# Performance work log

Hardware: AMD Instinct MI355X
Metric: run time of the kernel (lower is better)

## Reference

```python
import jax, jax.numpy as jnp
import numpy as np

TOP_K = 8
NUM_EXPERTS = 64


def setup_inputs() -> dict:
    key = jax.random.key(0)
    k1, k2 = jax.random.split(key)
    x = jax.random.normal(k1, (4, 4096, 2048), dtype=jnp.float32)
    # nn.Linear weight [num_experts, d_model], scaled like typical init
    gate_w = jax.random.normal(k2, (NUM_EXPERTS, 2048), dtype=jnp.float32) * 0.02
    expert_bias = jnp.zeros((NUM_EXPERTS,), dtype=jnp.float32)
    return {"x": x, "gate_w": gate_w, "expert_bias": expert_bias}


def reference(x, gate_w, expert_bias):
    # logits = gate(x): [b, s, E]
    logits = jnp.einsum("bsd,ed->bse", x, gate_w)
    # bias is detached in the original (routing-only, no grad)
    logits_with_bias = logits + jax.lax.stop_gradient(expert_bias)
    # top-k over experts
    top_k_logits, top_k_indices = jax.lax.top_k(logits_with_bias, TOP_K)
    # softmax over the small top-k dimension
    top_k_scores = jax.nn.softmax(top_k_logits, axis=-1)
    # scatter-add load counts per expert (training branch)
    flat_indices = top_k_indices.reshape(-1)
    expert_counts = jnp.zeros((NUM_EXPERTS,), dtype=jnp.int32).at[flat_indices].add(1)
    return top_k_scores, top_k_indices, expert_counts
```

## Files before the change

kernel.cpp:

```cpp
#include <hip/hip_runtime.h>
#include <math.h>

#define DIM   2048
#define NEXP  64
#define TOPK  8
#define ROWS  32
#define NT    512
#define KW    (DIM / 8)
#define STEPS (KW / 16)

typedef __attribute__((ext_vector_type(8)))  short bf16x8;
typedef __attribute__((ext_vector_type(16))) float f32x16;

#define MFMA(A, B, C) __builtin_amdgcn_mfma_f32_32x32x16_bf16(A, B, C, 0, 0, 0)
#define AS_BF(v) (*(const bf16x8*)&(v))

__device__ inline unsigned int bfpack(float a, float b) {
    unsigned int ua = __float_as_uint(a), ub = __float_as_uint(b);
    unsigned int lo = (ua + 0x7FFFu + ((ua >> 16) & 1u)) >> 16;
    unsigned int hi = (ub + 0x7FFFu + ((ub >> 16) & 1u)) & 0xFFFF0000u;
    return hi | lo;
}

__device__ inline void split2pair(float a, float b, unsigned int& h, unsigned int& m) {
    h = bfpack(a, b);
    float ra = a - __uint_as_float(h << 16);
    float rb = b - __uint_as_float(h & 0xFFFF0000u);
    m = bfpack(ra, rb);
}

__global__ __launch_bounds__(256) void prep_kernel(const float* __restrict__ w,
                                                   unsigned int* __restrict__ wpack,
                                                   float* __restrict__ counts) {
    const int t = blockIdx.x * 256 + threadIdx.x;
    if (blockIdx.x == 0 && threadIdx.x < NEXP) counts[threadIdx.x] = 0.0f;
    const float4 v0 = *(const float4*)(w + (size_t)t * 8);
    const float4 v1 = *(const float4*)(w + (size_t)t * 8 + 4);
    unsigned int h[4], m[4];
    split2pair(v0.x, v0.y, h[0], m[0]);
    split2pair(v0.z, v0.w, h[1], m[1]);
    split2pair(v1.x, v1.y, h[2], m[2]);
    split2pair(v1.z, v1.w, h[3], m[3]);
    uint4* dst = (uint4*)(wpack + (size_t)t * 8);
    dst[0] = (uint4){h[0], h[1], h[2], h[3]};
    dst[1] = (uint4){m[0], m[1], m[2], m[3]};
}

__global__ __launch_bounds__(NT, 4) void router_kernel(
    const float* __restrict__ x,
    const unsigned int* __restrict__ wpack,
    const float* __restrict__ bias,
    float* __restrict__ out,
    int M)
{
    __shared__ float lg[8][ROWS][NEXP + 2];
    __shared__ int   hist[NEXP];

    const int tid  = threadIdx.x;
    const int wv   = tid >> 6;
    const int lane = tid & 63;
    const int lrow = lane & 31;
    const int kh   = lane >> 5;
    const int row0 = blockIdx.x * ROWS;
    if (tid < NEXP) hist[tid] = 0;

    const float* xp = x + (size_t)(row0 + lrow) * DIM + wv * KW + kh * 8;
    const unsigned int* wb0 = wpack + ((size_t)lrow * (DIM / 8) + wv * (KW / 8) + kh) * 8;
    const unsigned int* wb1 = wb0 + (size_t)32 * (DIM / 8) * 8;

    f32x16 acc0 = {}, acc1 = {};

    #pragma unroll 4
    for (int t = 0; t < STEPS; ++t) {
        const float4 xv0 = *(const float4*)(xp + t * 16);
        const float4 xv1 = *(const float4*)(xp + t * 16 + 4);
        const uint4 b0h = *(const uint4*)(wb0 + (size_t)t * 16);
        const uint4 b0m = *(const uint4*)(wb0 + (size_t)t * 16 + 4);
        const uint4 b1h = *(const uint4*)(wb1 + (size_t)t * 16);
        const uint4 b1m = *(const uint4*)(wb1 + (size_t)t * 16 + 4);

        unsigned int ah[4], am[4];
        split2pair(xv0.x, xv0.y, ah[0], am[0]);
        split2pair(xv0.z, xv0.w, ah[1], am[1]);
        split2pair(xv1.x, xv1.y, ah[2], am[2]);
        split2pair(xv1.z, xv1.w, ah[3], am[3]);
        const uint4 ahv = (uint4){ah[0], ah[1], ah[2], ah[3]};
        const uint4 amv = (uint4){am[0], am[1], am[2], am[3]};

        acc0 = MFMA(AS_BF(ahv), AS_BF(b0h), acc0);
        acc1 = MFMA(AS_BF(ahv), AS_BF(b1h), acc1);
        acc0 = MFMA(AS_BF(amv), AS_BF(b0h), acc0);
        acc1 = MFMA(AS_BF(amv), AS_BF(b1h), acc1);
        acc0 = MFMA(AS_BF(ahv), AS_BF(b0m), acc0);
        acc1 = MFMA(AS_BF(ahv), AS_BF(b1m), acc1);
    }

    #pragma unroll
    for (int r = 0; r < 16; ++r) {
        const int rr = (r & 3) + 8 * (r >> 2) + 4 * kh;
        lg[wv][rr][lrow]      = acc0[r];
        lg[wv][rr][32 + lrow] = acc1[r];
    }
    __syncthreads();

    float* out_scores = out;
    float* out_idx    = out + (size_t)M * TOPK;
    float* out_counts = out + (size_t)2 * M * TOPK;

    #pragma unroll
    for (int i = 0; i < 4; ++i) {
        const int row = wv * 4 + i;
        float vm = bias[lane];
        #pragma unroll
        for (int p = 0; p < 8; ++p) vm += lg[p][row][lane];

        float vals[TOPK];
        int   ids[TOPK];
        #pragma unroll
        for (int k = 0; k < TOPK; ++k) {
            float mv = vm;
            int   mi = lane;
            #pragma unroll
            for (int off = 32; off > 0; off >>= 1) {
                float ov = __shfl_xor(mv, off);
                int   oi = __shfl_xor(mi, off);
                if (ov > mv || (ov == mv && oi < mi)) { mv = ov; mi = oi; }
            }
            vals[k] = mv; ids[k] = mi;
            if (lane == mi) { vm = -INFINITY; atomicAdd(&hist[mi], 1); }
        }
        if (lane == 0) {
            const float m = vals[0];
            float e[TOPK];
            float ssum = 0.f;
            #pragma unroll
            for (int k = 0; k < TOPK; ++k) { e[k] = expf(vals[k] - m); ssum += e[k]; }
            const float inv = 1.0f / ssum;
            const size_t base = (size_t)(row0 + row) * TOPK;
            #pragma unroll
            for (int k = 0; k < TOPK; ++k) {
                out_scores[base + k] = e[k] * inv;
                out_idx[base + k]    = (float)ids[k];
            }
        }
    }

    __syncthreads();
    if (tid < NEXP) atomicAdd(&out_counts[tid], (float)hist[tid]);
}

extern "C" void kernel_launch(void* const* d_in, const int* in_sizes, int n_in,
                              void* d_out, int out_size, void* d_ws, size_t ws_size,
                              hipStream_t stream) {
    const float* x    = (const float*)d_in[0];
    const float* w    = (const float*)d_in[1];
    const float* bias = (const float*)d_in[2];
    float* out = (float*)d_out;
    const int M = in_sizes[0] / DIM;

    unsigned int* wpack = (unsigned int*)d_ws;
    float* out_counts = out + (size_t)2 * M * TOPK;

    prep_kernel<<<(NEXP * DIM / 8) / 256, 256, 0, stream>>>(w, wpack, out_counts);
    router_kernel<<<M / ROWS, NT, 0, stream>>>(x, wpack, bias, out, M);
}
```

Before: 81.96 us.

## Stage x and packed weights through LDS with triple-buffered async global loads

```diff
diff --git a/kernel.cpp b/kernel.cpp
--- a/kernel.cpp
+++ b/kernel.cpp
@@ -1,19 +1,26 @@
 #include <hip/hip_runtime.h>
 #include <math.h>
 
-#define DIM   2048
-#define NEXP  64
-#define TOPK  8
-#define ROWS  32
-#define NT    512
-#define KW    (DIM / 8)
-#define STEPS (KW / 16)
+#define DIM    2048
+#define NEXP   64
+#define TOPK   8
+#define BM     64
+#define BK     64
+#define NT     512
+#define NTILES (DIM / BK)
+#define XTILE  (BM * BK * 4)
+#define WTILE  16384
 
 typedef __attribute__((ext_vector_type(8)))  short bf16x8;
 typedef __attribute__((ext_vector_type(16))) float f32x16;
 
 #define MFMA(A, B, C) __builtin_amdgcn_mfma_f32_32x32x16_bf16(A, B, C, 0, 0, 0)
 #define AS_BF(v) (*(const bf16x8*)&(v))
+
+typedef __attribute__((address_space(3))) unsigned int       lds_uint;
+typedef __attribute__((address_space(1))) const unsigned int glb_uint;
+#define GLOAD(gp, lp) __builtin_amdgcn_global_load_lds((glb_uint*)(const void*)(gp), \
+                                                       (lds_uint*)(void*)(lp), 16, 0, 0)
 
 __device__ inline unsigned int bfpack(float a, float b) {
     unsigned int ua = __float_as_uint(a), ub = __float_as_uint(b);
@@ -21,7 +28,6 @@
     unsigned int hi = (ub + 0x7FFFu + ((ub >> 16) & 1u)) & 0xFFFF0000u;
     return hi | lo;
 }
-
 __device__ inline void split2pair(float a, float b, unsigned int& h, unsigned int& m) {
     h = bfpack(a, b);
     float ra = a - __uint_as_float(h << 16);
@@ -32,74 +38,126 @@
 __global__ __launch_bounds__(256) void prep_kernel(const float* __restrict__ w,
                                                    unsigned int* __restrict__ wpack,
                                                    float* __restrict__ counts) {
-    const int t = blockIdx.x * 256 + threadIdx.x;
+    const int u = blockIdx.x * 256 + threadIdx.x;
     if (blockIdx.x == 0 && threadIdx.x < NEXP) counts[threadIdx.x] = 0.0f;
-    const float4 v0 = *(const float4*)(w + (size_t)t * 8);
-    const float4 v1 = *(const float4*)(w + (size_t)t * 8 + 4);
+    const int e = u >> 8, k8 = u & 255;
+    const float4 v0 = *(const float4*)(w + (size_t)e * DIM + k8 * 8);
+    const float4 v1 = *(const float4*)(w + (size_t)e * DIM + k8 * 8 + 4);
     unsigned int h[4], m[4];
     split2pair(v0.x, v0.y, h[0], m[0]);
     split2pair(v0.z, v0.w, h[1], m[1]);
     split2pair(v1.x, v1.y, h[2], m[2]);
     split2pair(v1.z, v1.w, h[3], m[3]);
-    uint4* dst = (uint4*)(wpack + (size_t)t * 8);
-    dst[0] = (uint4){h[0], h[1], h[2], h[3]};
-    dst[1] = (uint4){m[0], m[1], m[2], m[3]};
-}
-
-__global__ __launch_bounds__(NT, 4) void router_kernel(
+    const int kt = k8 >> 3, r3 = k8 & 7;
+    const int s = r3 >> 2, ks = (r3 >> 1) & 1, kh = r3 & 1;
+    const int c32 = e >> 5, e5 = e & 31;
+    char* base = (char*)wpack + (size_t)kt * WTILE + (kh << 9) + (e5 << 4);
+    *(uint4*)(base + (((((c32 * 2 + s) * 2 + ks) * 2) + 0) << 10)) = (uint4){h[0], h[1], h[2], h[3]};
+    *(uint4*)(base + (((((c32 * 2 + s) * 2 + ks) * 2) + 1) << 10)) = (uint4){m[0], m[1], m[2], m[3]};
+}
+
+__global__ __launch_bounds__(NT, 1) void router_kernel(
     const float* __restrict__ x,
     const unsigned int* __restrict__ wpack,
     const float* __restrict__ bias,
     float* __restrict__ out,
     int M)
 {
-    __shared__ float lg[8][ROWS][NEXP + 2];
-    __shared__ int   hist[NEXP];
+    __shared__ __align__(16) char xs[3][XTILE];
+    __shared__ __align__(16) char wsb[3][WTILE];
+    __shared__ int hist[NEXP];
 
     const int tid  = threadIdx.x;
     const int wv   = tid >> 6;
     const int lane = tid & 63;
-    const int lrow = lane & 31;
+    const int row0 = blockIdx.x * BM;
+    if (tid < NEXP) hist[tid] = 0;
+
+    const int Gd0 = wv * 64 + lane;
+    const int r0  = Gd0 >> 4, g0 = (Gd0 & 15) ^ (r0 & 7);
+    const int Gd1 = 512 + Gd0;
+    const int r1  = Gd1 >> 4, g1 = (Gd1 & 15) ^ (r1 & 7);
+    const float* xsrc0 = x + (size_t)(row0 + r0) * DIM + g0 * 4;
+    const float* xsrc1 = x + (size_t)(row0 + r1) * DIM + g1 * 4;
+    const unsigned int* wsrc = wpack + (wv << 8) + (lane << 2);
+
+#define STAGE(kt, b)                                              \
+    do {                                                          \
+        GLOAD(xsrc0 + (kt) * BK, &xs[b][(wv) << 10]);             \
+        GLOAD(xsrc1 + (kt) * BK, &xs[b][8192 + ((wv) << 10)]);    \
+        GLOAD(wsrc + (kt) * 4096, &wsb[b][(wv) << 10]);           \
+        GLOAD(wsrc + (kt) * 4096 + 2048, &wsb[b][8192 + ((wv) << 10)]); \
+    } while (0)
+
+    const int s    = wv >> 2;
+    const int tile = wv & 3;
+    const int trow = (tile >> 1) * 32;
+    const int c32  = tile & 1;
+    const int tcol = c32 * 32;
+    const int lr   = lane & 31;
     const int kh   = lane >> 5;
-    const int row0 = blockIdx.x * ROWS;
-    if (tid < NEXP) hist[tid] = 0;
-
-    const float* xp = x + (size_t)(row0 + lrow) * DIM + wv * KW + kh * 8;
-    const unsigned int* wb0 = wpack + ((size_t)lrow * (DIM / 8) + wv * (KW / 8) + kh) * 8;
-    const unsigned int* wb1 = wb0 + (size_t)32 * (DIM / 8) * 8;
-
-    f32x16 acc0 = {}, acc1 = {};
-
-    #pragma unroll 4
-    for (int t = 0; t < STEPS; ++t) {
-        const float4 xv0 = *(const float4*)(xp + t * 16);
-        const float4 xv1 = *(const float4*)(xp + t * 16 + 4);
-        const uint4 b0h = *(const uint4*)(wb0 + (size_t)t * 16);
-        const uint4 b0m = *(const uint4*)(wb0 + (size_t)t * 16 + 4);
-        const uint4 b1h = *(const uint4*)(wb1 + (size_t)t * 16);
-        const uint4 b1m = *(const uint4*)(wb1 + (size_t)t * 16 + 4);
-
-        unsigned int ah[4], am[4];
-        split2pair(xv0.x, xv0.y, ah[0], am[0]);
-        split2pair(xv0.z, xv0.w, ah[1], am[1]);
-        split2pair(xv1.x, xv1.y, ah[2], am[2]);
-        split2pair(xv1.z, xv1.w, ah[3], am[3]);
-        const uint4 ahv = (uint4){ah[0], ah[1], ah[2], ah[3]};
-        const uint4 amv = (uint4){am[0], am[1], am[2], am[3]};
-
-        acc0 = MFMA(AS_BF(ahv), AS_BF(b0h), acc0);
-        acc1 = MFMA(AS_BF(ahv), AS_BF(b1h), acc1);
-        acc0 = MFMA(AS_BF(amv), AS_BF(b0h), acc0);
-        acc1 = MFMA(AS_BF(amv), AS_BF(b1h), acc1);
-        acc0 = MFMA(AS_BF(ahv), AS_BF(b0m), acc0);
-        acc1 = MFMA(AS_BF(ahv), AS_BF(b1m), acc1);
-    }
-
-    #pragma unroll
-    for (int r = 0; r < 16; ++r) {
-        const int rr = (r & 3) + 8 * (r >> 2) + 4 * kh;
-        lg[wv][rr][lrow]      = acc0[r];
-        lg[wv][rr][32 + lrow] = acc1[r];
+    const int arow = trow + lr;
+    const int axor = arow & 7;
+    const int aoff = arow * 256;
+    const int wboff = (c32 * 2 + s) * 4096 + (kh << 9) + (lr << 4);
+    const float biasv = bias[tcol + lr];
+
+    f32x16 acc = {};
+
+    STAGE(0, 0); STAGE(1, 1); STAGE(2, 2);
+
+    for (int t = 0; t < NTILES; ++t) {
+        if (t < NTILES - 2)       asm volatile("s_waitcnt vmcnt(8)" ::: "memory");
+        else if (t == NTILES - 2) asm volatile("s_waitcnt vmcnt(4)" ::: "memory");
+        else                      asm volatile("s_waitcnt vmcnt(0)" ::: "memory");
+        __builtin_amdgcn_sched_barrier(0);
+        __builtin_amdgcn_s_barrier();
+
+        const int b = t % 3;
+        const char* xb = &xs[b][0];
+        const char* wb = &wsb[b][0];
+        #pragma unroll
+        for (int ks = 0; ks < 2; ++ks) {
+            const int ga = s * 8 + ks * 4 + kh * 2;
+            float4 a0 = *(const float4*)(xb + aoff + (((ga + 0) ^ axor) << 4));
+            float4 a1 = *(const float4*)(xb + aoff + (((ga + 1) ^ axor) << 4));
+            unsigned int ah[4], am[4];
+            split2pair(a0.x, a0.y, ah[0], am[0]);
+            split2pair(a0.z, a0.w, ah[1], am[1]);
+            split2pair(a1.x, a1.y, ah[2], am[2]);
+            split2pair(a1.z, a1.w, ah[3], am[3]);
+            const uint4 ahv = (uint4){ah[0], ah[1], ah[2], ah[3]};
+            const uint4 amv = (uint4){am[0], am[1], am[2], am[3]};
+            const uint4 bh = *(const uint4*)(wb + wboff + (ks << 11));
+            const uint4 bm = *(const uint4*)(wb + wboff + (ks << 11) + 1024);
+            acc = MFMA(AS_BF(ahv), AS_BF(bh), acc);
+            acc = MFMA(AS_BF(amv), AS_BF(bh), acc);
+            acc = MFMA(AS_BF(ahv), AS_BF(bm), acc);
+        }
+        asm volatile("s_waitcnt lgkmcnt(0)" ::: "memory");
+        __builtin_amdgcn_sched_barrier(0);
+        __builtin_amdgcn_s_barrier();
+        if (t + 3 < NTILES) STAGE(t + 3, b);
+    }
+
+    __syncthreads();
+
+    float* lg = (float*)&xs[0][0];
+    if (s == 0) {
+        #pragma unroll
+        for (int r = 0; r < 16; ++r) {
+            const int rr = (r & 3) + 8 * (r >> 2) + 4 * kh;
+            lg[(trow + rr) * 66 + tcol + lr] = acc[r];
+        }
+    }
+    __syncthreads();
+    if (s == 1) {
+        #pragma unroll
+        for (int r = 0; r < 16; ++r) {
+            const int rr = (r & 3) + 8 * (r >> 2) + 4 * kh;
+            const int idx = (trow + rr) * 66 + tcol + lr;
+            lg[idx] = lg[idx] + acc[r] + biasv;
+        }
     }
     __syncthreads();
 
@@ -107,13 +165,9 @@
     float* out_idx    = out + (size_t)M * TOPK;
     float* out_counts = out + (size_t)2 * M * TOPK;
 
-    #pragma unroll
-    for (int i = 0; i < 4; ++i) {
-        const int row = wv * 4 + i;
-        float vm = bias[lane];
-        #pragma unroll
-        for (int p = 0; p < 8; ++p) vm += lg[p][row][lane];
-
+    for (int r8 = 0; r8 < 8; ++r8) {
+        const int row = wv * 8 + r8;
+        float vm = lg[row * 66 + lane];
         float vals[TOPK];
         int   ids[TOPK];
         #pragma unroll
@@ -147,6 +201,7 @@
 
     __syncthreads();
     if (tid < NEXP) atomicAdd(&out_counts[tid], (float)hist[tid]);
+#undef STAGE
 }
 
 extern "C" void kernel_launch(void* const* d_in, const int* in_sizes, int n_in,
@@ -161,6 +216,6 @@
     unsigned int* wpack = (unsigned int*)d_ws;
     float* out_counts = out + (size_t)2 * M * TOPK;
 
-    prep_kernel<<<(NEXP * DIM / 8) / 256, 256, 0, stream>>>(w, wpack, out_counts);
-    router_kernel<<<M / ROWS, NT, 0, stream>>>(x, wpack, bias, out, M);
-}
+    prep_kernel<<<64, 256, 0, stream>>>(w, wpack, out_counts);
+    router_kernel<<<M / BM, NT, 0, stream>>>(x, wpack, bias, out, M);
+}
```

New measurement: 92.67 us. 13.1% more time.

## Repack gate weights per lane, prefetch loads two steps ahead, replace count atomics

Applied to the files above, without the earlier changes.

```diff
diff --git a/kernel.cpp b/kernel.cpp
--- a/kernel.cpp
+++ b/kernel.cpp
@@ -8,6 +8,7 @@
 #define NT    512
 #define KW    (DIM / 8)
 #define STEPS (KW / 16)
+#define NBLK  512
 
 typedef __attribute__((ext_vector_type(8)))  short bf16x8;
 typedef __attribute__((ext_vector_type(16))) float f32x16;
@@ -21,7 +22,6 @@
     unsigned int hi = (ub + 0x7FFFu + ((ub >> 16) & 1u)) & 0xFFFF0000u;
     return hi | lo;
 }
-
 __device__ inline void split2pair(float a, float b, unsigned int& h, unsigned int& m) {
     h = bfpack(a, b);
     float ra = a - __uint_as_float(h << 16);
@@ -30,20 +30,21 @@
 }
 
 __global__ __launch_bounds__(256) void prep_kernel(const float* __restrict__ w,
-                                                   unsigned int* __restrict__ wpack,
-                                                   float* __restrict__ counts) {
-    const int t = blockIdx.x * 256 + threadIdx.x;
-    if (blockIdx.x == 0 && threadIdx.x < NEXP) counts[threadIdx.x] = 0.0f;
-    const float4 v0 = *(const float4*)(w + (size_t)t * 8);
-    const float4 v1 = *(const float4*)(w + (size_t)t * 8 + 4);
+                                                   unsigned int* __restrict__ wpack) {
+    const int u = blockIdx.x * 256 + threadIdx.x;
+    const int e = u >> 8, k8 = u & 255;
+    const float4 v0 = *(const float4*)(w + (size_t)e * DIM + k8 * 8);
+    const float4 v1 = *(const float4*)(w + (size_t)e * DIM + k8 * 8 + 4);
     unsigned int h[4], m[4];
     split2pair(v0.x, v0.y, h[0], m[0]);
     split2pair(v0.z, v0.w, h[1], m[1]);
     split2pair(v1.x, v1.y, h[2], m[2]);
     split2pair(v1.z, v1.w, h[3], m[3]);
-    uint4* dst = (uint4*)(wpack + (size_t)t * 8);
-    dst[0] = (uint4){h[0], h[1], h[2], h[3]};
-    dst[1] = (uint4){m[0], m[1], m[2], m[3]};
+    const int lr = e & 31, c32 = e >> 5;
+    const int wv = k8 >> 5, r = k8 & 31, t = r >> 1, kh = r & 1;
+    char* base = (char*)wpack + ((((size_t)(lr * 2 + kh) * 8 + wv) * 16 + t) << 6) + c32 * 32;
+    *(uint4*)(base)      = (uint4){h[0], h[1], h[2], h[3]};
+    *(uint4*)(base + 16) = (uint4){m[0], m[1], m[2], m[3]};
 }
 
 __global__ __launch_bounds__(NT, 4) void router_kernel(
@@ -51,6 +52,7 @@
     const unsigned int* __restrict__ wpack,
     const float* __restrict__ bias,
     float* __restrict__ out,
+    int* __restrict__ histws,
     int M)
 {
     __shared__ float lg[8][ROWS][NEXP + 2];
@@ -59,53 +61,63 @@
     const int tid  = threadIdx.x;
     const int wv   = tid >> 6;
     const int lane = tid & 63;
-    const int lrow = lane & 31;
+    const int lr   = lane & 31;
     const int kh   = lane >> 5;
-    const int row0 = blockIdx.x * ROWS;
+    const int bid  = blockIdx.x;
+    const int swz  = (bid & 7) * (NBLK / 8) + (bid >> 3);
+    const int row0 = swz * ROWS;
     if (tid < NEXP) hist[tid] = 0;
 
-    const float* xp = x + (size_t)(row0 + lrow) * DIM + wv * KW + kh * 8;
-    const unsigned int* wb0 = wpack + ((size_t)lrow * (DIM / 8) + wv * (KW / 8) + kh) * 8;
-    const unsigned int* wb1 = wb0 + (size_t)32 * (DIM / 8) * 8;
+    const float* xp = x + (size_t)(row0 + lr) * DIM + wv * KW + kh * 8;
+    const char* wstream = (const char*)wpack + (((size_t)(lr * 2 + kh) * 8 + wv) << 10);
 
     f32x16 acc0 = {}, acc1 = {};
 
-    #pragma unroll 4
+    float4 xa[2], xb[2];
+    uint4  h0[2], m0[2], h1[2], m1[2];
+
+#define LOADSTEP(s, t)                                          \
+    do {                                                        \
+        xa[s] = *(const float4*)(xp + (t) * 16);                \
+        xb[s] = *(const float4*)(xp + (t) * 16 + 4);            \
+        const uint4* wp = (const uint4*)(wstream + (t) * 64);   \
+        h0[s] = wp[0]; m0[s] = wp[1]; h1[s] = wp[2]; m1[s] = wp[3]; \
+    } while (0)
+
+    LOADSTEP(0, 0);
+    LOADSTEP(1, 1);
+
+    #pragma unroll
     for (int t = 0; t < STEPS; ++t) {
-        const float4 xv0 = *(const float4*)(xp + t * 16);
-        const float4 xv1 = *(const float4*)(xp + t * 16 + 4);
-        const uint4 b0h = *(const uint4*)(wb0 + (size_t)t * 16);
-        const uint4 b0m = *(const uint4*)(wb0 + (size_t)t * 16 + 4);
-        const uint4 b1h = *(const uint4*)(wb1 + (size_t)t * 16);
-        const uint4 b1m = *(const uint4*)(wb1 + (size_t)t * 16 + 4);
-
+        const int s = t & 1;
         unsigned int ah[4], am[4];
-        split2pair(xv0.x, xv0.y, ah[0], am[0]);
-        split2pair(xv0.z, xv0.w, ah[1], am[1]);
-        split2pair(xv1.x, xv1.y, ah[2], am[2]);
-        split2pair(xv1.z, xv1.w, ah[3], am[3]);
+        split2pair(xa[s].x, xa[s].y, ah[0], am[0]);
+        split2pair(xa[s].z, xa[s].w, ah[1], am[1]);
+        split2pair(xb[s].x, xb[s].y, ah[2], am[2]);
+        split2pair(xb[s].z, xb[s].w, ah[3], am[3]);
         const uint4 ahv = (uint4){ah[0], ah[1], ah[2], ah[3]};
         const uint4 amv = (uint4){am[0], am[1], am[2], am[3]};
-
-        acc0 = MFMA(AS_BF(ahv), AS_BF(b0h), acc0);
-        acc1 = MFMA(AS_BF(ahv), AS_BF(b1h), acc1);
-        acc0 = MFMA(AS_BF(amv), AS_BF(b0h), acc0);
-        acc1 = MFMA(AS_BF(amv), AS_BF(b1h), acc1);
-        acc0 = MFMA(AS_BF(ahv), AS_BF(b0m), acc0);
-        acc1 = MFMA(AS_BF(ahv), AS_BF(b1m), acc1);
+        const uint4 bh0 = h0[s], bm0 = m0[s], bh1 = h1[s], bm1 = m1[s];
+        if (t + 2 < STEPS) LOADSTEP(s, t + 2);
+        acc0 = MFMA(AS_BF(ahv), AS_BF(bh0), acc0);
+        acc1 = MFMA(AS_BF(ahv), AS_BF(bh1), acc1);
+        acc0 = MFMA(AS_BF(amv), AS_BF(bh0), acc0);
+        acc1 = MFMA(AS_BF(amv), AS_BF(bh1), acc1);
+        acc0 = MFMA(AS_BF(ahv), AS_BF(bm0), acc0);
+        acc1 = MFMA(AS_BF(ahv), AS_BF(bm1), acc1);
     }
+#undef LOADSTEP
 
     #pragma unroll
     for (int r = 0; r < 16; ++r) {
         const int rr = (r & 3) + 8 * (r >> 2) + 4 * kh;
-        lg[wv][rr][lrow]      = acc0[r];
-        lg[wv][rr][32 + lrow] = acc1[r];
+        lg[wv][rr][lr]      = acc0[r];
+        lg[wv][rr][32 + lr] = acc1[r];
     }
     __syncthreads();
 
     float* out_scores = out;
     float* out_idx    = out + (size_t)M * TOPK;
-    float* out_counts = out + (size_t)2 * M * TOPK;
 
     #pragma unroll
     for (int i = 0; i < 4; ++i) {
@@ -146,7 +158,24 @@
     }
 
     __syncthreads();
-    if (tid < NEXP) atomicAdd(&out_counts[tid], (float)hist[tid]);
+    if (tid < NEXP) histws[bid * NEXP + tid] = hist[tid];
+}
+
+__global__ __launch_bounds__(512) void reduce_kernel(const int* __restrict__ histws,
+                                                     float* __restrict__ counts) {
+    __shared__ int part[8][NEXP];
+    const int t = threadIdx.x;
+    const int e = t & 63, c = t >> 6;
+    int s = 0;
+    for (int b = c; b < NBLK; b += 8) s += histws[b * NEXP + e];
+    part[c][e] = s;
+    __syncthreads();
+    if (t < NEXP) {
+        int tot = 0;
+        #pragma unroll
+        for (int i = 0; i < 8; ++i) tot += part[i][t];
+        counts[t] = (float)tot;
+    }
 }
 
 extern "C" void kernel_launch(void* const* d_in, const int* in_sizes, int n_in,
@@ -159,8 +188,10 @@
     const int M = in_sizes[0] / DIM;
 
     unsigned int* wpack = (unsigned int*)d_ws;
+    int* histws = (int*)((char*)d_ws + (size_t)NEXP * DIM * 4);
     float* out_counts = out + (size_t)2 * M * TOPK;
 
-    prep_kernel<<<(NEXP * DIM / 8) / 256, 256, 0, stream>>>(w, wpack, out_counts);
-    router_kernel<<<M / ROWS, NT, 0, stream>>>(x, wpack, bias, out, M);
+    prep_kernel<<<64, 256, 0, stream>>>(w, wpack);
+    router_kernel<<<NBLK, NT, 0, stream>>>(x, wpack, bias, out, histws, M);
+    reduce_kernel<<<1, 512, 0, stream>>>(histws, out_counts);
 }
```

Result: slower. 92.14 us (+12.4%).
